# Performance work log

Hardware: AMD Instinct MI355X
Metric: run time of the kernel (lower is better)

Reference implementation:

```python
import jax, jax.numpy as jnp
import numpy as np

H = 3072; NH = 24; HD = 128; MLP_D = 12288
B = 1; IMG = 1536; REF = 512; TXT = 256

def _gelu_tanh(x):
    return jax.nn.gelu(x, approximate=True)

def _ln(x, eps=1e-6):
    m = jnp.mean(x, axis=-1, keepdims=True)
    v = jnp.var(x, axis=-1, keepdims=True)
    return (x - m) * jax.lax.rsqrt(v + eps)

def _rms(x, g, eps=1e-6):
    return x * jax.lax.rsqrt(jnp.mean(x * x, axis=-1, keepdims=True) + eps) * g

def _rot_half(x):
    # interleaved rotate-half: (x0,x1,x2,x3,...) -> (-x1,x0,-x3,x2,...)
    x2 = x.reshape(x.shape[:-1] + (-1, 2))
    return jnp.stack([-x2[..., 1], x2[..., 0]], axis=-1).reshape(x.shape)

def setup_inputs():
    key = jax.random.key(0)
    ks = jax.random.split(key, 16)
    s = 0.02
    # rope tables for image tokens (interleaved layout, values repeated x2)
    inv_freq = 1.0 / (10000.0 ** (jnp.arange(0, HD // 2, dtype=jnp.float32) / (HD // 2)))
    ang = jnp.arange(IMG, dtype=jnp.float32)[:, None] * inv_freq[None, :]   # [IMG, HD//2]
    ang = jnp.repeat(ang, 2, axis=-1)                                       # [IMG, HD]
    return {
        'x':   jax.random.normal(ks[0], (B, IMG + TXT, H), jnp.float32),
        'vec': jax.random.normal(ks[1], (B, H), jnp.float32),
        'ref': jax.random.normal(ks[2], (B, REF, H), jnp.float32),
        'cos': jnp.cos(ang), 'sin': jnp.sin(ang),
        'mod_w':  jax.random.normal(ks[3], (H, 3 * H), jnp.float32) * s,
        'mod_b':  jnp.zeros((3 * H,), jnp.float32),
        'rf1_w':  jax.random.normal(ks[4], (H, H), jnp.float32) * s,
        'rf1_b':  jnp.zeros((H,), jnp.float32),
        'rf2_w':  jax.random.normal(ks[5], (H, H), jnp.float32) * s,
        'rf2_b':  jnp.zeros((H,), jnp.float32),
        'rln_g':  jnp.ones((H,), jnp.float32),
        'rln_b':  jnp.zeros((H,), jnp.float32),
        'lin1_w': jax.random.normal(ks[6], (H, 3 * H + MLP_D), jnp.float32) * s,
        'lin1_b': jnp.zeros((3 * H + MLP_D,), jnp.float32),
        'q_g':    jnp.ones((HD,), jnp.float32),
        'k_g':    jnp.ones((HD,), jnp.float32),
        'lin2_w': jax.random.normal(ks[7], (H + MLP_D, H), jnp.float32) * s,
        'lin2_b': jnp.zeros((H,), jnp.float32),
        'text_mask': jnp.ones((B, TXT), jnp.int32),
        'img_len': IMG, 'txt_len': TXT,
    }

def _forward(x, vec, ref, cos, sin, mod_w, mod_b, rf1_w, rf1_b, rf2_w, rf2_b,
             rln_g, rln_b, lin1_w, lin1_b, q_g, k_g, lin2_w, lin2_b,
             text_mask, img_len, txt_len):
    Bb = x.shape[0]
    ref_len = ref.shape[1]
    # modulation (ModulateDiT: SiLU -> Linear -> chunk(3))
    mod = jnp.dot(jax.nn.silu(vec), mod_w) + mod_b
    shift, scale, gate = jnp.split(mod, 3, axis=-1)
    x_mod = _ln(x) * (1.0 + scale[:, None]) + shift[:, None]
    # ref MLP + affine LayerNorm
    r = jnp.dot(_gelu_tanh(jnp.dot(ref, rf1_w) + rf1_b), rf2_w) + rf2_b
    r = _ln(r) * rln_g + rln_b
    # token reassembly: [img | ref | txt]
    xc = jnp.concatenate([x_mod[:, :img_len], r, x_mod[:, img_len:]], axis=1)
    h = jnp.dot(xc, lin1_w) + lin1_b
    qkv, mlp = h[..., :3 * H], h[..., 3 * H:]
    L2 = xc.shape[1]
    q, k, v = [t.reshape(Bb, L2, NH, HD) for t in jnp.split(qkv, 3, axis=-1)]
    # q drops the ref span; ref contributes K/V only
    q = jnp.concatenate([q[:, :img_len], q[:, img_len + ref_len:]], axis=1)
    q = _rms(q, q_g)
    k = _rms(k, k_g)
    # rotary only on image tokens
    c = cos[None, :, None, :]; s = sin[None, :, None, :]
    img_q = q[:, :img_len] * c + _rot_half(q[:, :img_len]) * s
    img_k = k[:, :img_len] * c + _rot_half(k[:, :img_len]) * s
    q = jnp.concatenate([img_q, q[:, img_len:]], axis=1)          # [B, Lq, NH, HD]
    k = jnp.concatenate([img_k, k[:, img_len:]], axis=1)          # [B, Lkv, NH, HD]
    # varlen mask (cu_seqlens semantics): valid attends valid, pad attends pad
    tmask = text_mask.astype(bool)
    qv  = jnp.concatenate([jnp.ones((Bb, img_len), bool), tmask], axis=1)
    kvv = jnp.concatenate([jnp.ones((Bb, img_len + ref_len), bool), tmask], axis=1)
    allowed = (qv[:, None, :, None] == kvv[:, None, None, :])     # [B,1,Lq,Lkv]
    scores = jnp.einsum('bqhd,bkhd->bhqk', q, k) * (HD ** -0.5)
    scores = jnp.where(allowed, scores, jnp.asarray(-1e9, scores.dtype))
    p = jax.nn.softmax(scores, axis=-1)
    attn = jnp.einsum('bhqk,bkhd->bqhd', p, v).reshape(Bb, img_len + txt_len, H)
    mlp = jnp.concatenate([mlp[:, :img_len], mlp[:, img_len + ref_len:]], axis=1)
    out = jnp.dot(jnp.concatenate([attn, _gelu_tanh(mlp)], axis=-1), lin2_w) + lin2_b
    return x + out * gate[:, None]

def reference(x, vec, ref, cos, sin, mod_w, mod_b, rf1_w, rf1_b, rf2_w, rf2_b,
              rln_g, rln_b, lin1_w, lin1_b, q_g, k_g, lin2_w, lin2_b,
              text_mask, img_len, txt_len):
    return _forward(x, vec, ref, cos, sin, mod_w, mod_b, rf1_w, rf1_b, rf2_w, rf2_b,
                    rln_g, rln_b, lin1_w, lin1_b, q_g, k_g, lin2_w, lin2_b,
                    text_mask, img_len, txt_len)
```

## Files before the change

### kernel.cpp

```cpp
#include <hip/hip_runtime.h>
#include <cstdint>
#include <cstddef>

typedef unsigned short u16;
typedef unsigned int   u32;
typedef __bf16 bf16_t;
typedef bf16_t bf16x8 __attribute__((ext_vector_type(8)));
typedef float  f32x4  __attribute__((ext_vector_type(4)));
typedef u16    u16x4  __attribute__((ext_vector_type(4)));


__device__ __forceinline__ float b2f(u16 b){ u32 u=((u32)b)<<16; float f; __builtin_memcpy(&f,&u,4); return f; }
__device__ __forceinline__ u16 f2b(float f){ u32 u; __builtin_memcpy(&u,&f,4); u = u + 0x7fffu + ((u>>16)&1u); return (u16)(u>>16); }
__device__ __forceinline__ float gelu_f(float x){
  const float u2 = 1.5957691216057308f*(x + 0.044715f*x*x*x);
  return x/(1.f + __expf(-u2));
}

__device__ __forceinline__ void gload_lds16(const void* g, void* l){
  __builtin_amdgcn_global_load_lds((const __attribute__((address_space(1))) void*)g,
                                   (__attribute__((address_space(3))) void*)l, 16, 0, 0);
}

template<int NW, bool MX>
__device__ __forceinline__ float bred(float v, float* red){
  #pragma unroll
  for (int o=32;o;o>>=1){ float u=__shfl_down(v,o,64); v = MX? fmaxf(v,u) : v+u; }
  const int t = threadIdx.x;
  if ((t&63)==0) red[t>>6]=v;
  __syncthreads();
  float r = red[0];
  #pragma unroll
  for (int i=1;i<NW;i++) r = MX? fmaxf(r,red[i]) : r+red[i];
  __syncthreads();
  return r;
}

__device__ __forceinline__ void unpack8(uint4 u, float* f){
  f[0]=b2f((u16)(u.x&0xffffu)); f[1]=b2f((u16)(u.x>>16));
  f[2]=b2f((u16)(u.y&0xffffu)); f[3]=b2f((u16)(u.y>>16));
  f[4]=b2f((u16)(u.z&0xffffu)); f[5]=b2f((u16)(u.z>>16));
  f[6]=b2f((u16)(u.w&0xffffu)); f[7]=b2f((u16)(u.w>>16));
}
__device__ __forceinline__ uint4 pack8(const float* f){
  uint4 u;
  u.x = (u32)f2b(f[0]) | ((u32)f2b(f[1])<<16);
  u.y = (u32)f2b(f[2]) | ((u32)f2b(f[3])<<16);
  u.z = (u32)f2b(f[4]) | ((u32)f2b(f[5])<<16);
  u.w = (u32)f2b(f[6]) | ((u32)f2b(f[7])<<16);
  return u;
}

__global__ void modv_part(const float* __restrict__ vec, const float* __restrict__ W,
                          float* __restrict__ part){
  __shared__ float s[128];
  const int t = threadIdx.x;
  const int j = blockIdx.x*256 + t;
  const int i0 = blockIdx.y*128;
  if (t < 128){ float v = vec[i0+t]; s[t] = v/(1.f+__expf(-v)); }
  __syncthreads();
  float acc = 0.f;
  #pragma unroll 8
  for (int i=0;i<128;i++) acc += s[i]*W[(size_t)(i0+i)*9216 + j];
  part[(size_t)blockIdx.y*9216 + j] = acc;
}
__global__ void modv_reduce(const float* __restrict__ part, const float* __restrict__ mb,
                            float* __restrict__ modp){
  const int j = blockIdx.x*256 + threadIdx.x;
  float a = mb[j];
  #pragma unroll
  for (int c=0;c<24;c++) a += part[(size_t)c*9216 + j];
  modp[j] = a;
}

__global__ __launch_bounds__(256)
void convT(const float* __restrict__ W, u16* __restrict__ Wt, int Kd, int Nd){
  __shared__ float Ls[64][65];
  const int t = threadIdx.x;
  const int n0 = blockIdx.x*64, k0 = blockIdx.y*64;
  const int tr = t>>4;
  const int tc = (t&15)*4;
  #pragma unroll
  for (int p=0;p<4;p++){
    const int kk = tr + p*16;
    const float4 v = *(const float4*)(W + (size_t)(k0+kk)*Nd + n0 + tc);
    Ls[kk][tc+0]=v.x; Ls[kk][tc+1]=v.y; Ls[kk][tc+2]=v.z; Ls[kk][tc+3]=v.w;
  }
  __syncthreads();
  #pragma unroll
  for (int p=0;p<4;p++){
    const int nn = tr + p*16;
    u16x4 o;
    o.x = f2b(Ls[tc+0][nn]); o.y = f2b(Ls[tc+1][nn]);
    o.z = f2b(Ls[tc+2][nn]); o.w = f2b(Ls[tc+3][nn]);
    *(u16x4*)(Wt + (size_t)(n0+nn)*Kd + k0 + tc) = o;
  }
}

__global__ void convertF2B(const float* __restrict__ src, u16* __restrict__ dst){
  const size_t i = ((size_t)blockIdx.x*256 + threadIdx.x)*4;
  const float4 v = *(const float4*)(src+i);
  u16x4 o; o.x=f2b(v.x); o.y=f2b(v.y); o.z=f2b(v.z); o.w=f2b(v.w);
  *(u16x4*)(dst+i) = o;
}

__global__ void ln_modulate(const float* __restrict__ x, const float* __restrict__ modp,
                            u16* __restrict__ xc){
  __shared__ float red[4];
  const int row = blockIdx.x, t = threadIdx.x;
  const float* xr = x + (size_t)row*3072;
  float4 v[3]; float s=0.f, ss=0.f;
  #pragma unroll
  for (int k=0;k<3;k++){
    v[k] = *(const float4*)(xr + t*4 + k*1024);
    s  += v[k].x+v[k].y+v[k].z+v[k].w;
    ss += v[k].x*v[k].x+v[k].y*v[k].y+v[k].z*v[k].z+v[k].w*v[k].w;
  }
  s  = bred<4,false>(s, red);
  ss = bred<4,false>(ss, red);
  const float mean = s*(1.f/3072.f);
  const float inv = rsqrtf(ss*(1.f/3072.f)-mean*mean + 1e-6f);
  const int orow = row<1536 ? row : row+512;
  u16* o = xc + (size_t)orow*3072;
  const float* shiftp = modp; const float* scalep = modp+3072;
  #pragma unroll
  for (int k=0;k<3;k++){
    const int j = t*4 + k*1024;
    const float4 sc = *(const float4*)(scalep+j);
    const float4 sh = *(const float4*)(shiftp+j);
    u16x4 ov;
    ov.x = f2b((v[k].x-mean)*inv*(1.f+sc.x)+sh.x);
    ov.y = f2b((v[k].y-mean)*inv*(1.f+sc.y)+sh.y);
    ov.z = f2b((v[k].z-mean)*inv*(1.f+sc.z)+sh.z);
    ov.w = f2b((v[k].w-mean)*inv*(1.f+sc.w)+sh.w);
    *(u16x4*)(o+j) = ov;
  }
}

__global__ void ln_ref(const float* __restrict__ rt, const float* __restrict__ g,
                       const float* __restrict__ b, u16* __restrict__ xc){
  __shared__ float red[4];
  const int row = blockIdx.x, t = threadIdx.x;
  const float* xr = rt + (size_t)row*3072;
  float4 v[3]; float s=0.f, ss=0.f;
  #pragma unroll
  for (int k=0;k<3;k++){
    v[k] = *(const float4*)(xr + t*4 + k*1024);
    s  += v[k].x+v[k].y+v[k].z+v[k].w;
    ss += v[k].x*v[k].x+v[k].y*v[k].y+v[k].z*v[k].z+v[k].w*v[k].w;
  }
  s  = bred<4,false>(s, red);
  ss = bred<4,false>(ss, red);
  const float mean = s*(1.f/3072.f);
  const float inv = rsqrtf(ss*(1.f/3072.f)-mean*mean + 1e-6f);
  u16* o = xc + (size_t)(1536+row)*3072;
  #pragma unroll
  for (int k=0;k<3;k++){
    const int j = t*4 + k*1024;
    const float4 gv = *(const float4*)(g+j);
    const float4 bv = *(const float4*)(b+j);
    u16x4 ov;
    ov.x = f2b((v[k].x-mean)*inv*gv.x+bv.x);
    ov.y = f2b((v[k].y-mean)*inv*gv.y+bv.y);
    ov.z = f2b((v[k].z-mean)*inv*gv.z+bv.z);
    ov.w = f2b((v[k].w-mean)*inv*gv.w+bv.w);
    *(u16x4*)(o+j) = ov;
  }
}

__global__ void qk_prep(const u16* __restrict__ h, const float* __restrict__ qg,
                        const float* __restrict__ kg, const float* __restrict__ cosb,
                        const float* __restrict__ sinb, u16* __restrict__ Q,
                        u16* __restrict__ Kb){
  __shared__ float red[4];
  const int row = blockIdx.x, hd = blockIdx.y, d = threadIdx.x;
  const u16* hr = h + (size_t)row*21504;
  const float kv = b2f(hr[3072 + hd*128 + d]);
  const bool doq = (row < 1536) || (row >= 2048);
  const float qv = doq ? b2f(hr[hd*128 + d]) : 0.f;
  float a = kv*kv, b = qv*qv;
  #pragma unroll
  for (int o=32;o;o>>=1){ a += __shfl_down(a,o,64); b += __shfl_down(b,o,64); }
  if ((d&63)==0){ red[(d>>6)*2] = a; red[(d>>6)*2+1] = b; }
  __syncthreads();
  const float kinv = rsqrtf((red[0]+red[2])*(1.f/128.f) + 1e-6f);
  const float qinv = rsqrtf((red[1]+red[3])*(1.f/128.f) + 1e-6f);
  float kn = kv*kinv*kg[d];
  float qn = qv*qinv*qg[d];
  if (row < 1536){
    const float c  = cosb[row*128 + d];
    const float sn = sinb[row*128 + d];
    const float ko = b2f(hr[3072 + hd*128 + (d^1)])*kinv*kg[d^1];
    const float qo = b2f(hr[hd*128 + (d^1)])*qinv*qg[d^1];
    const float krh = (d&1) ? ko : -ko;
    const float qrh = (d&1) ? qo : -qo;
    kn = kn*c + krh*sn;
    qn = qn*c + qrh*sn;
  }
  Kb[((size_t)hd*2304 + row)*128 + d] = f2b(kn);
  if (doq){
    const int qrow = row<1536 ? row : row-512;
    Q[((size_t)hd*1792 + qrow)*128 + d] = f2b(qn);
  }
}

__global__ void v_transpose(const u16* __restrict__ h, u16* __restrict__ VT){
  __shared__ u16 Ls[32][33];
  const int tx = threadIdx.x, ty = threadIdx.y;
  const int l0 = blockIdx.x*32, d0 = blockIdx.y*32, hd = blockIdx.z;
  #pragma unroll
  for (int r=0;r<4;r++)
    Ls[ty+r*8][tx] = h[(size_t)(l0+ty+r*8)*21504 + 6144 + hd*128 + d0 + tx];
  __syncthreads();
  #pragma unroll
  for (int r=0;r<4;r++)
    VT[((size_t)hd*128 + d0+ty+r*8)*2304 + l0 + tx] = Ls[tx][ty+r*8];
}

__global__ void gelu_mlp(const u16* __restrict__ h, u16* __restrict__ out2){
  const int q = blockIdx.x;
  const int hrow = q<1536 ? q : q+512;
  const int j = blockIdx.y*2048 + threadIdx.x*8;
  const uint4 u = *(const uint4*)(h + (size_t)hrow*21504 + 9216 + j);
  float f[8]; unpack8(u, f);
  #pragma unroll
  for (int e=0;e<8;e++) f[e] = gelu_f(f[e]);
  const uint4 o = pack8(f);
  *(uint4*)(out2 + (size_t)q*15360 + 3072 + j) = o;
}

template<int EPI>
__global__ __launch_bounds__(256)
void gemm_bt(const u16* __restrict__ A, const u16* __restrict__ Bt,
             const float* __restrict__ bias, void* __restrict__ Cv,
             int K, int ldA, int ldB, int ldC,
             long long sA, long long sB, long long sC)
{
  __shared__ u16 As[128*32];
  __shared__ u16 Bs[128*32];
  const int t = threadIdx.x;
  const int w = t>>6, lane = t&63;
  const int bm = blockIdx.y, bn = blockIdx.x, bz = blockIdx.z;
  const u16* Ab = A + (size_t)((long long)bz*sA) + (size_t)bm*128*ldA;
  const u16* Bb = Bt + (size_t)((long long)bz*sB) + (size_t)bn*128*ldB;
  const int wm = w>>1, wn = w&1;
  const int lr = lane&15, lk = lane>>4;
  const int row0 = t>>2, kp0 = (t&3)*8;
  char* AsB = (char*)As; char* BsB = (char*)Bs;
  const int off0 = w*1024;
  const int off1 = 4096 + w*1024;
  f32x4 acc[4][4] = {};

  for (int kt = 0; kt < K; kt += 32){
    __syncthreads();
    gload_lds16(Ab + (size_t)row0*ldA + kt + kp0,      AsB + off0);
    gload_lds16(Ab + (size_t)(row0+64)*ldA + kt + kp0, AsB + off1);
    gload_lds16(Bb + (size_t)row0*ldB + kt + kp0,      BsB + off0);
    gload_lds16(Bb + (size_t)(row0+64)*ldB + kt + kp0, BsB + off1);
    __syncthreads();
    bf16x8 av[4], bv[4];
    #pragma unroll
    for (int i=0;i<4;i++) av[i] = *(const bf16x8*)(As + (wm*64+i*16+lr)*32 + lk*8);
    #pragma unroll
    for (int j=0;j<4;j++) bv[j] = *(const bf16x8*)(Bs + (wn*64+j*16+lr)*32 + lk*8);
    #pragma unroll
    for (int i=0;i<4;i++)
      #pragma unroll
      for (int j=0;j<4;j++)
        acc[i][j] = __builtin_amdgcn_mfma_f32_16x16x32_bf16(av[i], bv[j], acc[i][j], 0,0,0);
  }

  const int mBase = bm*128 + wm*64;
  const int nBase = bn*128 + wn*64;
  #pragma unroll
  for (int i=0;i<4;i++){
    #pragma unroll
    for (int j=0;j<4;j++){
      #pragma unroll
      for (int r=0;r<4;r++){
        const int m = mBase + i*16 + lk*4 + r;
        const int n = nBase + j*16 + lr;
        const float v = acc[i][j][r];
        const long long idx = (long long)bz*sC + (long long)m*ldC + n;
        if (EPI==6){
          ((float*)Cv)[idx] = v;
        } else {
          ((u16*)Cv)[idx] = f2b(v + bias[n]);
        }
      }
    }
  }
}

__global__ void comb_gelu(const float* __restrict__ P, const float* __restrict__ b,
                          u16* __restrict__ o){
  const size_t e = ((size_t)blockIdx.x*256 + threadIdx.x)*4;
  const int n = (int)(e % 3072);
  const size_t S = (size_t)512*3072;
  float4 a = *(const float4*)(P + e);
  #pragma unroll
  for (int c=1;c<6;c++){
    const float4 p = *(const float4*)(P + c*S + e);
    a.x+=p.x; a.y+=p.y; a.z+=p.z; a.w+=p.w;
  }
  const float4 bb = *(const float4*)(b + n);
  u16x4 ov;
  ov.x = f2b(gelu_f(a.x+bb.x)); ov.y = f2b(gelu_f(a.y+bb.y));
  ov.z = f2b(gelu_f(a.z+bb.z)); ov.w = f2b(gelu_f(a.w+bb.w));
  *(u16x4*)(o + e) = ov;
}
__global__ void comb_bias(const float* __restrict__ P, const float* __restrict__ b,
                          float* __restrict__ o){
  const size_t e = ((size_t)blockIdx.x*256 + threadIdx.x)*4;
  const int n = (int)(e % 3072);
  const size_t S = (size_t)512*3072;
  float4 a = *(const float4*)(P + e);
  #pragma unroll
  for (int c=1;c<6;c++){
    const float4 p = *(const float4*)(P + c*S + e);
    a.x+=p.x; a.y+=p.y; a.z+=p.z; a.w+=p.w;
  }
  const float4 bb = *(const float4*)(b + n);
  float4 ov; ov.x=a.x+bb.x; ov.y=a.y+bb.y; ov.z=a.z+bb.z; ov.w=a.w+bb.w;
  *(float4*)(o + e) = ov;
}

#define G256_BAR()  __builtin_amdgcn_s_barrier()
#define G256_LGKM() do{ asm volatile("s_waitcnt lgkmcnt(0)" ::: "memory"); \
                        __builtin_amdgcn_sched_barrier(0); }while(0)

template<int CEPI>
__global__ __launch_bounds__(512,2)
void gemm256(const u16* __restrict__ A, const u16* __restrict__ Bt,
             const float* __restrict__ bias, void* __restrict__ Cv,
             int Kc, int ld, int ldC, int nbn, int ntile, long long sC, int nwg, int gm)
{
  __shared__ char smem[131072];
  const int t = threadIdx.x;
  const int wid = t>>6, lane = t&63;
  const int lr = lane&15, lk = lane>>4;
  const int wm = wid>>2, wn = wid&3;

  const int orig = blockIdx.x;
  const int q8 = nwg>>3, r8 = nwg&7;
  const int xcd = orig&7, jj = orig>>3;
  const int wg = (xcd<r8 ? xcd*(q8+1) : r8*(q8+1) + (xcd-r8)*q8) + jj;
  int sk, bm, bn;
  if (gm > 0){
    const int band = wg / (gm*nbn);
    const int rr = wg - band*(gm*nbn);
    bn = rr / gm;
    bm = band*gm + (rr - bn*gm);
    sk = 0;
  } else {
    sk = wg / ntile;
    const int rem = wg - sk*ntile;
    bm = rem / nbn; bn = rem % nbn;
  }

  const u16* Agl = A  + (size_t)bm*256*ld + (size_t)sk*Kc;
  const u16* Bgl = Bt + (size_t)bn*256*ld + (size_t)sk*Kc;
  const int NT = Kc>>6;

  const int d0 = wid*64 + lane;
  const int sr = d0>>3;
  const size_t soff = (size_t)sr*ld + (size_t)(((d0&7)^(sr&7))<<3);

  const int xsl0 = ((lk    ) ^ (lr&7))<<4;
  const int xsl1 = ((lk | 4) ^ (lr&7))<<4;

  f32x4 acc[8][4] = {};
  bf16x8 bv[4][2];

  auto STAGE = [&](const u16* g, int h, int kt, char* ldsMat){
    const u16* s0 = g + (size_t)(h*128)*ld + kt + soff;
    char* l0 = ldsMat + h*16384 + wid*1024;
    gload_lds16(s0, l0);
    gload_lds16(s0 + (size_t)64*ld, l0 + 8192);
  };

  STAGE(Agl, 0, 0, smem);
  STAGE(Agl, 1, 0, smem);
  STAGE(Bgl, 0, 0, smem + 32768);
  STAGE(Bgl, 1, 0, smem + 32768);
  if (NT > 1){
    STAGE(Bgl, 0, 64, smem + 65536 + 32768);
    STAGE(Bgl, 1, 64, smem + 65536 + 32768);
    asm volatile("s_waitcnt vmcnt(4)" ::: "memory");
  } else {
    asm volatile("s_waitcnt vmcnt(0)" ::: "memory");
  }
  G256_BAR();

#define G256_MFMA_Q(Q)                                                          \
  do{                                                                           \
    _Pragma("unroll")                                                           \
    for (int j=0;j<4;j++){                                                      \
      acc[(Q)*2+0][j] = __builtin_amdgcn_mfma_f32_16x16x32_bf16(av00, bv[j][0], acc[(Q)*2+0][j], 0,0,0); \
      acc[(Q)*2+0][j] = __builtin_amdgcn_mfma_f32_16x16x32_bf16(av01, bv[j][1], acc[(Q)*2+0][j], 0,0,0); \
      acc[(Q)*2+1][j] = __builtin_amdgcn_mfma_f32_16x16x32_bf16(av10, bv[j][0], acc[(Q)*2+1][j], 0,0,0); \
      acc[(Q)*2+1][j] = __builtin_amdgcn_mfma_f32_16x16x32_bf16(av11, bv[j][1], acc[(Q)*2+1][j], 0,0,0); \
    }                                                                           \
  }while(0)

#define G256_PHASE(Q, STG, TAILW)                                               \
  do{                                                                           \
    const char* abase = cA + (wm*128 + (Q)*32 + lr)*128;                        \
    bf16x8 av00 = *(const bf16x8*)(abase + xsl0);                               \
    bf16x8 av01 = *(const bf16x8*)(abase + xsl1);                               \
    bf16x8 av10 = *(const bf16x8*)(abase + 2048 + xsl0);                        \
    bf16x8 av11 = *(const bf16x8*)(abase + 2048 + xsl1);                        \
    if ((Q)==0){                                                                \
      _Pragma("unroll")                                                         \
      for (int j=0;j<4;j++){                                                    \
        const char* bbase = cB + (wn*64 + j*16 + lr)*128;                       \
        bv[j][0] = *(const bf16x8*)(bbase + xsl0);                              \
        bv[j][1] = *(const bf16x8*)(bbase + xsl1);                              \
      }                                                                         \
    }                                                                           \
    STG;                                                                        \
    G256_BAR();                                                                 \
    G256_LGKM();                                                                \
    __builtin_amdgcn_s_setprio(1);                                              \
    G256_MFMA_Q(Q);                                                             \
    __builtin_amdgcn_s_setprio(0);                                              \
    TAILW;                                                                      \
    G256_BAR();                                                                 \
  }while(0)

  for (int tt = 0; tt < NT; ++tt){
    char* cA = smem + (tt&1)*65536;
    char* cB = cA + 32768;
    char* nA = smem + ((tt+1)&1)*65536;
    const int kt1 = (tt+1)<<6, kt2 = (tt+2)<<6;
    const bool stA = (tt+1) < NT, stB = (tt+2) < NT;

    G256_PHASE(0, if (stA) STAGE(Agl, 0, kt1, nA), );
    G256_PHASE(1, if (stA) STAGE(Agl, 1, kt1, nA), );
    G256_PHASE(2, if (stB) STAGE(Bgl, 0, kt2, cB), );
    G256_PHASE(3, if (stB) STAGE(Bgl, 1, kt2, cB),
               if (stB)      { asm volatile("s_waitcnt vmcnt(4)" ::: "memory"); }
               else if (stA) { asm volatile("s_waitcnt vmcnt(0)" ::: "memory"); } );
  }
#undef G256_PHASE
#undef G256_MFMA_Q

  const int mB = bm*256 + wm*128 + lk*4;
  const int nB = bn*256 + wn*64 + lr;
  #pragma unroll
  for (int fi=0; fi<8; fi++){
    #pragma unroll
    for (int j=0; j<4; j++){
      const int n = nB + j*16;
      const float bb = (CEPI==0) ? bias[n] : 0.f;
      #pragma unroll
      for (int r=0;r<4;r++){
        const int m = mB + fi*16 + r;
        if (CEPI==0){
          ((u16*)Cv)[(size_t)m*ldC + n] = f2b(acc[fi][j][r] + bb);
        } else {
          ((float*)Cv)[(size_t)sk*sC + (size_t)m*ldC + n] = acc[fi][j][r];
        }
      }
    }
  }
}

__global__ __launch_bounds__(512)
void flash_attn(const u16* __restrict__ Qb, const u16* __restrict__ Kb,
                const u16* __restrict__ VT, const int* __restrict__ tmask,
                u16* __restrict__ out2)
{
  __shared__ __attribute__((aligned(16))) char smf[81920];
  char* Ks0 = smf;
  char* Vs0 = smf + 32768;
  char* Ps  = smf + 65536;
  const int t = threadIdx.x, wid = t>>6, lane = t&63;
  const int lr = lane&15, hi = lane>>4;
  const int head = blockIdx.y, qt = blockIdx.x;
  const int q0 = qt*128;
  const u16* Qg = Qb + ((size_t)head*1792 + q0)*128;
  const u16* Kg = Kb + (size_t)head*2304*128;
  const u16* Vg = VT + (size_t)head*128*2304;
  const float SCALE = 0.08838834764831845f;

  u32 kbits = 0;
  #pragma unroll
  for (int i=0;i<16;i++) kbits |= (u32)(tmask[i*16 + lr] != 0) << i;
  int fqr[4];
  #pragma unroll
  for (int r=0;r<4;r++){
    const int q = q0 + wid*16 + hi*4 + r;
    fqr[r] = (q < 1536) ? 1 : (tmask[q-1536] != 0);
  }

  #pragma unroll
  for (int c=0;c<4;c++){
    const int s = c*512 + wid*64 + lane;
    const int row = s>>4, dsl = s&15;
    gload_lds16(Qg + (size_t)row*128 + ((dsl ^ (row&7))<<3),
                Vs0 + (size_t)(c*512 + wid*64)*16);
  }
  #pragma unroll
  for (int c=0;c<2;c++){
    const int s = c*512 + wid*64 + lane;
    const int row = s>>4, dsl = s&15;
    gload_lds16(Kg + (size_t)row*128 + ((dsl ^ (row&7))<<3),
                Ks0 + (size_t)(c*512 + wid*64)*16);
  }
  asm volatile("s_waitcnt vmcnt(0)" ::: "memory");
  __syncthreads();

  bf16x8 av[4];
  {
    const int row = wid*16 + lr;
    #pragma unroll
    for (int ks=0;ks<4;ks++)
      av[ks] = *(const bf16x8*)(Vs0 + row*256 + (((ks*4+hi) ^ (row&7))<<4));
  }
  asm volatile("s_waitcnt lgkmcnt(0)" ::: "memory");
  __builtin_amdgcn_sched_barrier(0);
  __syncthreads();

  #pragma unroll
  for (int c=0;c<2;c++){
    const int s = c*512 + wid*64 + lane;
    const int row = s>>3, dsl = s&7;
    gload_lds16(Vg + (size_t)row*2304 + ((dsl ^ (row&7))<<3),
                Vs0 + (size_t)(c*512 + wid*64)*16);
  }
  asm volatile("s_waitcnt vmcnt(0)" ::: "memory");
  __syncthreads();

  f32x4 acc[8] = {};
  float m_[4], l_[4];
  #pragma unroll
  for (int r=0;r<4;r++){ m_[r] = -3e38f; l_[r] = 0.f; }

  for (int kt = 0; kt < 36; ++kt){
    char* Kc = Ks0 + (kt&1)*16384;
    char* Vc = Vs0 + (kt&1)*16384;
    if (kt+1 < 36){
      char* Kn = Ks0 + ((kt+1)&1)*16384;
      char* Vn = Vs0 + ((kt+1)&1)*16384;
      #pragma unroll
      for (int c=0;c<2;c++){
        const int s = c*512 + wid*64 + lane;
        { const int row = s>>4, dsl = s&15;
          gload_lds16(Kg + (size_t)((kt+1)*64 + row)*128 + ((dsl ^ (row&7))<<3),
                      Kn + (size_t)(c*512 + wid*64)*16); }
        { const int row = s>>3, dsl = s&7;
          gload_lds16(Vg + (size_t)row*2304 + (kt+1)*64 + ((dsl ^ (row&7))<<3),
                      Vn + (size_t)(c*512 + wid*64)*16); }
      }
    }
    f32x4 sacc[4] = {};
    #pragma unroll
    for (int ks=0;ks<4;ks++){
      #pragma unroll
      for (int j=0;j<4;j++){
        const int row = j*16 + lr;
        bf16x8 bk = *(const bf16x8*)(Kc + row*256 + (((ks*4+hi) ^ (row&7))<<4));
        sacc[j] = __builtin_amdgcn_mfma_f32_16x16x32_bf16(av[ks], bk, sacc[j], 0,0,0);
      }
    }
    int gkj[4];
    #pragma unroll
    for (int j=0;j<4;j++)
      gkj[j] = (kt < 32) ? 1 : (int)((kbits >> ((kt-32)*4 + j)) & 1u);
    float p[4][4]; bool alw[4][4];
    float mt[4] = {-3e38f,-3e38f,-3e38f,-3e38f};
    #pragma unroll
    for (int j=0;j<4;j++){
      #pragma unroll
      for (int r=0;r<4;r++){
        const float s = sacc[j][r]*SCALE;
        const bool a = (fqr[r] == gkj[j]);
        alw[j][r] = a; p[j][r] = s;
        if (a) mt[r] = fmaxf(mt[r], s);
      }
    }
    #pragma unroll
    for (int r=0;r<4;r++){
      #pragma unroll
      for (int o=1;o<16;o<<=1) mt[r] = fmaxf(mt[r], __shfl_xor(mt[r], o, 64));
      const float nm = fmaxf(m_[r], mt[r]);
      const float cr = __expf(m_[r] - nm);
      m_[r] = nm;
      l_[r] *= cr;
      #pragma unroll
      for (int jp=0;jp<8;jp++) acc[jp][r] *= cr;
    }
    float rs[4] = {0.f,0.f,0.f,0.f};
    #pragma unroll
    for (int j=0;j<4;j++){
      #pragma unroll
      for (int r=0;r<4;r++){
        const float pv = alw[j][r] ? __expf(p[j][r] - m_[r]) : 0.f;
        p[j][r] = pv; rs[r] += pv;
      }
    }
    #pragma unroll
    for (int r=0;r<4;r++){
      #pragma unroll
      for (int o=1;o<16;o<<=1) rs[r] += __shfl_xor(rs[r], o, 64);
      l_[r] += rs[r];
    }
    #pragma unroll
    for (int j=0;j<4;j++){
      #pragma unroll
      for (int r=0;r<4;r++){
        const int q = wid*16 + hi*4 + r;
        const int k = j*16 + lr;
        *(u16*)(Ps + q*128 + (((k>>3) ^ (q&7))<<4) + (k&7)*2) = f2b(p[j][r]);
      }
    }
    asm volatile("s_waitcnt lgkmcnt(0)" ::: "memory");
    __builtin_amdgcn_sched_barrier(0);
    bf16x8 pa[2];
    {
      const int row = wid*16 + lr;
      #pragma unroll
      for (int ks2=0;ks2<2;ks2++)
        pa[ks2] = *(const bf16x8*)(Ps + row*128 + (((ks2*4+hi) ^ (row&7))<<4));
    }
    #pragma unroll
    for (int ks2=0;ks2<2;ks2++){
      #pragma unroll
      for (int jp=0;jp<8;jp++){
        const int row = jp*16 + lr;
        bf16x8 bvv = *(const bf16x8*)(Vc + row*128 + (((ks2*4+hi) ^ (row&7))<<4));
        acc[jp] = __builtin_amdgcn_mfma_f32_16x16x32_bf16(pa[ks2], bvv, acc[jp], 0,0,0);
      }
    }
    asm volatile("s_waitcnt vmcnt(0)" ::: "memory");
    __syncthreads();
  }

  float inv[4];
  #pragma unroll
  for (int r=0;r<4;r++) inv[r] = 1.f/l_[r];
  #pragma unroll
  for (int jp=0;jp<8;jp++){
    #pragma unroll
    for (int r=0;r<4;r++){
      const size_t q = q0 + wid*16 + hi*4 + r;
      out2[q*15360 + head*128 + jp*16 + lr] = f2b(acc[jp][r]*inv[r]);
    }
  }
}

__global__ void lin2_fin(const float* __restrict__ P, const float* __restrict__ x,
                         const float* __restrict__ bias, const float* __restrict__ gate,
                         float* __restrict__ out){
  const size_t e = ((size_t)blockIdx.x*256 + threadIdx.x)*4;
  const int n = (int)(e % 3072);
  const size_t S = (size_t)1792*3072;
  float4 a = *(const float4*)(P + e);
  #pragma unroll
  for (int c=1;c<6;c++){
    const float4 p = *(const float4*)(P + c*S + e);
    a.x+=p.x; a.y+=p.y; a.z+=p.z; a.w+=p.w;
  }
  const float4 bb = *(const float4*)(bias + n);
  const float4 gg = *(const float4*)(gate + n);
  const float4 xv = *(const float4*)(x + e);
  float4 o;
  o.x = xv.x + (a.x+bb.x)*gg.x;
  o.y = xv.y + (a.y+bb.y)*gg.y;
  o.z = xv.z + (a.z+bb.z)*gg.z;
  o.w = xv.w + (a.w+bb.w)*gg.w;
  *(float4*)(out + e) = o;
}

extern "C" void kernel_launch(void* const* d_in, const int* in_sizes, int n_in,
                              void* d_out, int out_size, void* d_ws, size_t ws_size,
                              hipStream_t stream)
{
  (void)in_sizes; (void)n_in; (void)out_size; (void)ws_size;
  const float* x     = (const float*)d_in[0];
  const float* vec   = (const float*)d_in[1];
  const float* ref   = (const float*)d_in[2];
  const float* cosb  = (const float*)d_in[3];
  const float* sinb  = (const float*)d_in[4];
  const float* mod_w = (const float*)d_in[5];
  const float* mod_b = (const float*)d_in[6];
  const float* rf1_w = (const float*)d_in[7];
  const float* rf1_b = (const float*)d_in[8];
  const float* rf2_w = (const float*)d_in[9];
  const float* rf2_b = (const float*)d_in[10];
  const float* rln_g = (const float*)d_in[11];
  const float* rln_b = (const float*)d_in[12];
  const float* lin1_w= (const float*)d_in[13];
  const float* lin1_b= (const float*)d_in[14];
  const float* q_g   = (const float*)d_in[15];
  const float* k_g   = (const float*)d_in[16];
  const float* lin2_w= (const float*)d_in[17];
  const float* lin2_b= (const float*)d_in[18];
  const int*   tmask = (const int*)d_in[19];
  float* out = (float*)d_out;
  char* ws = (char*)d_ws;

  float* modp = (float*)(ws + 0);
  float* part = (float*)(ws + 36864);
  u16*  w2t   = (u16*)(ws + 921600);
  u16*  Qb    = (u16*)(ws + 95293440ll);
  u16*  Kb    = (u16*)(ws + 106303488ll);
  u16*  VT    = (u16*)(ws + 120459264ll);
  u16*  out2  = (u16*)(ws + 134615040ll);
  u16*  w1t   = (u16*)(ws + 189665280ll);
  u16*  xc    = (u16*)(ws + 321785856ll);
  u16*  rf1t  = (u16*)(ws + 335941632ll);
  u16*  rf2t  = (u16*)(ws + 354816000ll);
  u16*  refb  = (u16*)(ws + 373690368ll);
  u16*  tb    = (u16*)(ws + 376836096ll);
  float* rtmp = (float*)(ws + 379981824ll);
  float* rp   = (float*)(ws + 386273280ll);
  u16*  hbuf  = (u16*)(ws + 335941632ll);
  float* p2b  = (float*)(ws + 189665280ll);

  modv_part<<<dim3(36,24),256,0,stream>>>(vec, mod_w, part);
  modv_reduce<<<36,256,0,stream>>>(part, mod_b, modp);
  convT<<<dim3(48,48),  256,0,stream>>>(rf1_w, rf1t, 3072, 3072);
  convT<<<dim3(48,48),  256,0,stream>>>(rf2_w, rf2t, 3072, 3072);
  convT<<<dim3(336,48), 256,0,stream>>>(lin1_w, w1t, 3072, 21504);
  convT<<<dim3(48,240), 256,0,stream>>>(lin2_w, w2t, 15360, 3072);
  convertF2B<<<1536,256,0,stream>>>(ref, refb);
  ln_modulate<<<1792,256,0,stream>>>(x, modp, xc);
  gemm_bt<6><<<dim3(24,4,6),256,0,stream>>>(refb, rf1t, nullptr, rp, 512, 3072,3072,3072,
                                            512,512, (long long)512*3072);
  comb_gelu<<<1536,256,0,stream>>>(rp, rf1_b, tb);
  gemm_bt<6><<<dim3(24,4,6),256,0,stream>>>(tb, rf2t, nullptr, rp, 512, 3072,3072,3072,
                                            512,512, (long long)512*3072);
  comb_bias<<<1536,256,0,stream>>>(rp, rf2_b, rtmp);
  ln_ref<<<512,256,0,stream>>>(rtmp, rln_g, rln_b, xc);
  gemm256<0><<<756,512,0,stream>>>(xc, w1t, lin1_b, hbuf, 3072, 3072, 21504, 84, 756, 0, 756, 3);
  gelu_mlp<<<dim3(1792,6),256,0,stream>>>(hbuf, out2);
  qk_prep<<<dim3(2304,24),128,0,stream>>>(hbuf, q_g, k_g, cosb, sinb, Qb, Kb);
  v_transpose<<<dim3(72,4,24),dim3(32,8),0,stream>>>(hbuf, VT);
  flash_attn<<<dim3(14,24),512,0,stream>>>(Qb, Kb, VT, tmask, out2);
  gemm256<1><<<504,512,0,stream>>>(out2, w2t, nullptr, p2b, 2560, 15360, 3072, 12, 84,
                                   (long long)1792*3072, 504, 0);
  lin2_fin<<<5376,256,0,stream>>>(p2b, x, lin2_b, modp + 6144, out);
}
```

Baseline: 923.7 us.

## Merge GEMM k-loop into two phases and bound flash_attn occupancy

Restructures the 256x256 GEMM main loop from four phases (each with two barriers) into two phases that each load two A sub-tiles and issue both A stages or both B stages at once, halving the barrier count per k-step. It also adds a min-blocks hint of 4 to the flash_attention launch bounds. The merged phases hold more A fragments live, which raises register pressure. The launch-bounds hint may force register spilling in the attention kernel.

```diff
diff --git a/kernel.cpp b/kernel.cpp
--- a/kernel.cpp
+++ b/kernel.cpp
@@ -392,42 +392,6 @@
   }
   G256_BAR();
 
-#define G256_MFMA_Q(Q)                                                          \
-  do{                                                                           \
-    _Pragma("unroll")                                                           \
-    for (int j=0;j<4;j++){                                                      \
-      acc[(Q)*2+0][j] = __builtin_amdgcn_mfma_f32_16x16x32_bf16(av00, bv[j][0], acc[(Q)*2+0][j], 0,0,0); \
-      acc[(Q)*2+0][j] = __builtin_amdgcn_mfma_f32_16x16x32_bf16(av01, bv[j][1], acc[(Q)*2+0][j], 0,0,0); \
-      acc[(Q)*2+1][j] = __builtin_amdgcn_mfma_f32_16x16x32_bf16(av10, bv[j][0], acc[(Q)*2+1][j], 0,0,0); \
-      acc[(Q)*2+1][j] = __builtin_amdgcn_mfma_f32_16x16x32_bf16(av11, bv[j][1], acc[(Q)*2+1][j], 0,0,0); \
-    }                                                                           \
-  }while(0)
-
-#define G256_PHASE(Q, STG, TAILW)                                               \
-  do{                                                                           \
-    const char* abase = cA + (wm*128 + (Q)*32 + lr)*128;                        \
-    bf16x8 av00 = *(const bf16x8*)(abase + xsl0);                               \
-    bf16x8 av01 = *(const bf16x8*)(abase + xsl1);                               \
-    bf16x8 av10 = *(const bf16x8*)(abase + 2048 + xsl0);                        \
-    bf16x8 av11 = *(const bf16x8*)(abase + 2048 + xsl1);                        \
-    if ((Q)==0){                                                                \
-      _Pragma("unroll")                                                         \
-      for (int j=0;j<4;j++){                                                    \
-        const char* bbase = cB + (wn*64 + j*16 + lr)*128;                       \
-        bv[j][0] = *(const bf16x8*)(bbase + xsl0);                              \
-        bv[j][1] = *(const bf16x8*)(bbase + xsl1);                              \
-      }                                                                         \
-    }                                                                           \
-    STG;                                                                        \
-    G256_BAR();                                                                 \
-    G256_LGKM();                                                                \
-    __builtin_amdgcn_s_setprio(1);                                              \
-    G256_MFMA_Q(Q);                                                             \
-    __builtin_amdgcn_s_setprio(0);                                              \
-    TAILW;                                                                      \
-    G256_BAR();                                                                 \
-  }while(0)
-
   for (int tt = 0; tt < NT; ++tt){
     char* cA = smem + (tt&1)*65536;
     char* cB = cA + 32768;
@@ -435,15 +399,73 @@
     const int kt1 = (tt+1)<<6, kt2 = (tt+2)<<6;
     const bool stA = (tt+1) < NT, stB = (tt+2) < NT;
 
-    G256_PHASE(0, if (stA) STAGE(Agl, 0, kt1, nA), );
-    G256_PHASE(1, if (stA) STAGE(Agl, 1, kt1, nA), );
-    G256_PHASE(2, if (stB) STAGE(Bgl, 0, kt2, cB), );
-    G256_PHASE(3, if (stB) STAGE(Bgl, 1, kt2, cB),
-               if (stB)      { asm volatile("s_waitcnt vmcnt(4)" ::: "memory"); }
-               else if (stA) { asm volatile("s_waitcnt vmcnt(0)" ::: "memory"); } );
-  }
-#undef G256_PHASE
-#undef G256_MFMA_Q
+    {
+      const char* ab0 = cA + (wm*128 + 0*32 + lr)*128;
+      const char* ab1 = cA + (wm*128 + 1*32 + lr)*128;
+      bf16x8 a00 = *(const bf16x8*)(ab0 + xsl0);
+      bf16x8 a01 = *(const bf16x8*)(ab0 + xsl1);
+      bf16x8 a02 = *(const bf16x8*)(ab0 + 2048 + xsl0);
+      bf16x8 a03 = *(const bf16x8*)(ab0 + 2048 + xsl1);
+      bf16x8 a10 = *(const bf16x8*)(ab1 + xsl0);
+      bf16x8 a11 = *(const bf16x8*)(ab1 + xsl1);
+      bf16x8 a12 = *(const bf16x8*)(ab1 + 2048 + xsl0);
+      bf16x8 a13 = *(const bf16x8*)(ab1 + 2048 + xsl1);
+      #pragma unroll
+      for (int j=0;j<4;j++){
+        const char* bbase = cB + (wn*64 + j*16 + lr)*128;
+        bv[j][0] = *(const bf16x8*)(bbase + xsl0);
+        bv[j][1] = *(const bf16x8*)(bbase + xsl1);
+      }
+      if (stA){ STAGE(Agl, 0, kt1, nA); STAGE(Agl, 1, kt1, nA); }
+      G256_BAR();
+      G256_LGKM();
+      __builtin_amdgcn_s_setprio(1);
+      #pragma unroll
+      for (int j=0;j<4;j++){
+        acc[0][j] = __builtin_amdgcn_mfma_f32_16x16x32_bf16(a00, bv[j][0], acc[0][j], 0,0,0);
+        acc[0][j] = __builtin_amdgcn_mfma_f32_16x16x32_bf16(a01, bv[j][1], acc[0][j], 0,0,0);
+        acc[1][j] = __builtin_amdgcn_mfma_f32_16x16x32_bf16(a02, bv[j][0], acc[1][j], 0,0,0);
+        acc[1][j] = __builtin_amdgcn_mfma_f32_16x16x32_bf16(a03, bv[j][1], acc[1][j], 0,0,0);
+        acc[2][j] = __builtin_amdgcn_mfma_f32_16x16x32_bf16(a10, bv[j][0], acc[2][j], 0,0,0);
+        acc[2][j] = __builtin_amdgcn_mfma_f32_16x16x32_bf16(a11, bv[j][1], acc[2][j], 0,0,0);
+        acc[3][j] = __builtin_amdgcn_mfma_f32_16x16x32_bf16(a12, bv[j][0], acc[3][j], 0,0,0);
+        acc[3][j] = __builtin_amdgcn_mfma_f32_16x16x32_bf16(a13, bv[j][1], acc[3][j], 0,0,0);
+      }
+      __builtin_amdgcn_s_setprio(0);
+      G256_BAR();
+    }
+    {
+      const char* ab2 = cA + (wm*128 + 2*32 + lr)*128;
+      const char* ab3 = cA + (wm*128 + 3*32 + lr)*128;
+      bf16x8 a20 = *(const bf16x8*)(ab2 + xsl0);
+      bf16x8 a21 = *(const bf16x8*)(ab2 + xsl1);
+      bf16x8 a22 = *(const bf16x8*)(ab2 + 2048 + xsl0);
+      bf16x8 a23 = *(const bf16x8*)(ab2 + 2048 + xsl1);
+      bf16x8 a30 = *(const bf16x8*)(ab3 + xsl0);
+      bf16x8 a31 = *(const bf16x8*)(ab3 + xsl1);
+      bf16x8 a32 = *(const bf16x8*)(ab3 + 2048 + xsl0);
+      bf16x8 a33 = *(const bf16x8*)(ab3 + 2048 + xsl1);
+      if (stB){ STAGE(Bgl, 0, kt2, cB); STAGE(Bgl, 1, kt2, cB); }
+      G256_BAR();
+      G256_LGKM();
+      __builtin_amdgcn_s_setprio(1);
+      #pragma unroll
+      for (int j=0;j<4;j++){
+        acc[4][j] = __builtin_amdgcn_mfma_f32_16x16x32_bf16(a20, bv[j][0], acc[4][j], 0,0,0);
+        acc[4][j] = __builtin_amdgcn_mfma_f32_16x16x32_bf16(a21, bv[j][1], acc[4][j], 0,0,0);
+        acc[5][j] = __builtin_amdgcn_mfma_f32_16x16x32_bf16(a22, bv[j][0], acc[5][j], 0,0,0);
+        acc[5][j] = __builtin_amdgcn_mfma_f32_16x16x32_bf16(a23, bv[j][1], acc[5][j], 0,0,0);
+        acc[6][j] = __builtin_amdgcn_mfma_f32_16x16x32_bf16(a30, bv[j][0], acc[6][j], 0,0,0);
+        acc[6][j] = __builtin_amdgcn_mfma_f32_16x16x32_bf16(a31, bv[j][1], acc[6][j], 0,0,0);
+        acc[7][j] = __builtin_amdgcn_mfma_f32_16x16x32_bf16(a32, bv[j][0], acc[7][j], 0,0,0);
+        acc[7][j] = __builtin_amdgcn_mfma_f32_16x16x32_bf16(a33, bv[j][1], acc[7][j], 0,0,0);
+      }
+      __builtin_amdgcn_s_setprio(0);
+      if (stB)      { asm volatile("s_waitcnt vmcnt(4)" ::: "memory"); }
+      else if (stA) { asm volatile("s_waitcnt vmcnt(0)" ::: "memory"); }
+      G256_BAR();
+    }
+  }
 
   const int mB = bm*256 + wm*128 + lk*4;
   const int nB = bn*256 + wn*64 + lr;
@@ -466,7 +488,7 @@
   }
 }
 
-__global__ __launch_bounds__(512)
+__global__ __launch_bounds__(512,4)
 void flash_attn(const u16* __restrict__ Qb, const u16* __restrict__ Kb,
                 const u16* __restrict__ VT, const int* __restrict__ tmask,
                 u16* __restrict__ out2)
```

Result: no change. 906.6 us (-1.8%).

## Skip unused lin1 tiles for ref rows and unroll GEMM K-loop by two

Applied to the files above, without the earlier changes.

Adds a custom tile map for the lin1 GEMM. For the reference-token row blocks it launches only the column tiles that produce K and V, skipping the Q and MLP outputs that are later discarded. This cuts the grid from 756 to 636 workgroups. The gemm256 main loop is also unrolled over two K-steps with fixed LDS buffer pointers, which removes per-iteration buffer address arithmetic but assumes an even number of K tiles. flash_attn gets a min-blocks hint of 4 in its launch bounds, which may constrain register allocation.

```diff
diff --git a/kernel.cpp b/kernel.cpp
--- a/kernel.cpp
+++ b/kernel.cpp
@@ -328,6 +328,20 @@
 #define G256_BAR()  __builtin_amdgcn_s_barrier()
 #define G256_LGKM() do{ asm volatile("s_waitcnt lgkmcnt(0)" ::: "memory"); \
                         __builtin_amdgcn_sched_barrier(0); }while(0)
+#define G256_VM4()  asm volatile("s_waitcnt vmcnt(4)" ::: "memory")
+#define G256_VM0()  asm volatile("s_waitcnt vmcnt(0)" ::: "memory")
+
+__device__ __forceinline__ void lin1_map(int tw, int& bm, int& bn){
+  if (tw < 504){
+    const int band = tw/252; const int rr = tw - band*252;
+    bn = rr/3; bm = band*3 + (rr - bn*3);
+  } else if (tw < 588){
+    bm = 8; bn = tw - 504;
+  } else {
+    const int rem = tw - 588;
+    bm = 6 + (rem&1); bn = 12 + (rem>>1);
+  }
+}
 
 template<int CEPI>
 __global__ __launch_bounds__(512,2)
@@ -346,7 +360,9 @@
   const int xcd = orig&7, jj = orig>>3;
   const int wg = (xcd<r8 ? xcd*(q8+1) : r8*(q8+1) + (xcd-r8)*q8) + jj;
   int sk, bm, bn;
-  if (gm > 0){
+  if (gm == -1){
+    sk = 0; lin1_map(wg, bm, bn);
+  } else if (gm > 0){
     const int band = wg / (gm*nbn);
     const int rr = wg - band*(gm*nbn);
     bn = rr / gm;
@@ -361,13 +377,18 @@
   const u16* Agl = A  + (size_t)bm*256*ld + (size_t)sk*Kc;
   const u16* Bgl = Bt + (size_t)bn*256*ld + (size_t)sk*Kc;
   const int NT = Kc>>6;
+  const int NI = NT>>1;
 
   const int d0 = wid*64 + lane;
   const int sr = d0>>3;
   const size_t soff = (size_t)sr*ld + (size_t)(((d0&7)^(sr&7))<<3);
-
   const int xsl0 = ((lk    ) ^ (lr&7))<<4;
   const int xsl1 = ((lk | 4) ^ (lr&7))<<4;
+
+  char* s0A = smem;
+  char* s0B = smem + 32768;
+  char* s1A = smem + 65536;
+  char* s1B = smem + 98304;
 
   f32x4 acc[8][4] = {};
   bf16x8 bv[4][2];
@@ -379,71 +400,62 @@
     gload_lds16(s0 + (size_t)64*ld, l0 + 8192);
   };
 
-  STAGE(Agl, 0, 0, smem);
-  STAGE(Agl, 1, 0, smem);
-  STAGE(Bgl, 0, 0, smem + 32768);
-  STAGE(Bgl, 1, 0, smem + 32768);
-  if (NT > 1){
-    STAGE(Bgl, 0, 64, smem + 65536 + 32768);
-    STAGE(Bgl, 1, 64, smem + 65536 + 32768);
-    asm volatile("s_waitcnt vmcnt(4)" ::: "memory");
-  } else {
-    asm volatile("s_waitcnt vmcnt(0)" ::: "memory");
-  }
+  STAGE(Agl, 0, 0, s0A);
+  STAGE(Agl, 1, 0, s0A);
+  STAGE(Bgl, 0, 0, s0B);
+  STAGE(Bgl, 1, 0, s0B);
+  STAGE(Bgl, 0, 64, s1B);
+  STAGE(Bgl, 1, 64, s1B);
+  G256_VM4();
   G256_BAR();
 
-#define G256_MFMA_Q(Q)                                                          \
+#define G256_PH(SA, Q, READB, SB, STG, TAILV)                                   \
   do{                                                                           \
-    _Pragma("unroll")                                                           \
-    for (int j=0;j<4;j++){                                                      \
-      acc[(Q)*2+0][j] = __builtin_amdgcn_mfma_f32_16x16x32_bf16(av00, bv[j][0], acc[(Q)*2+0][j], 0,0,0); \
-      acc[(Q)*2+0][j] = __builtin_amdgcn_mfma_f32_16x16x32_bf16(av01, bv[j][1], acc[(Q)*2+0][j], 0,0,0); \
-      acc[(Q)*2+1][j] = __builtin_amdgcn_mfma_f32_16x16x32_bf16(av10, bv[j][0], acc[(Q)*2+1][j], 0,0,0); \
-      acc[(Q)*2+1][j] = __builtin_amdgcn_mfma_f32_16x16x32_bf16(av11, bv[j][1], acc[(Q)*2+1][j], 0,0,0); \
-    }                                                                           \
-  }while(0)
-
-#define G256_PHASE(Q, STG, TAILW)                                               \
-  do{                                                                           \
-    const char* abase = cA + (wm*128 + (Q)*32 + lr)*128;                        \
-    bf16x8 av00 = *(const bf16x8*)(abase + xsl0);                               \
-    bf16x8 av01 = *(const bf16x8*)(abase + xsl1);                               \
-    bf16x8 av10 = *(const bf16x8*)(abase + 2048 + xsl0);                        \
-    bf16x8 av11 = *(const bf16x8*)(abase + 2048 + xsl1);                        \
-    if ((Q)==0){                                                                \
+    const char* ab = SA + (wm*128 + (Q)*32 + lr)*128;                           \
+    bf16x8 a0 = *(const bf16x8*)(ab + xsl0);                                    \
+    bf16x8 a1 = *(const bf16x8*)(ab + xsl1);                                    \
+    bf16x8 a2 = *(const bf16x8*)(ab + 2048 + xsl0);                             \
+    bf16x8 a3 = *(const bf16x8*)(ab + 2048 + xsl1);                             \
+    if (READB){                                                                 \
       _Pragma("unroll")                                                         \
       for (int j=0;j<4;j++){                                                    \
-        const char* bbase = cB + (wn*64 + j*16 + lr)*128;                       \
-        bv[j][0] = *(const bf16x8*)(bbase + xsl0);                              \
-        bv[j][1] = *(const bf16x8*)(bbase + xsl1);                              \
+        const char* bb = SB + (wn*64 + j*16 + lr)*128;                          \
+        bv[j][0] = *(const bf16x8*)(bb + xsl0);                                 \
+        bv[j][1] = *(const bf16x8*)(bb + xsl1);                                 \
       }                                                                         \
     }                                                                           \
     STG;                                                                        \
     G256_BAR();                                                                 \
     G256_LGKM();                                                                \
     __builtin_amdgcn_s_setprio(1);                                              \
-    G256_MFMA_Q(Q);                                                             \
+    _Pragma("unroll")                                                           \
+    for (int j=0;j<4;j++){                                                      \
+      acc[(Q)*2+0][j] = __builtin_amdgcn_mfma_f32_16x16x32_bf16(a0, bv[j][0], acc[(Q)*2+0][j], 0,0,0); \
+      acc[(Q)*2+0][j] = __builtin_amdgcn_mfma_f32_16x16x32_bf16(a1, bv[j][1], acc[(Q)*2+0][j], 0,0,0); \
+      acc[(Q)*2+1][j] = __builtin_amdgcn_mfma_f32_16x16x32_bf16(a2, bv[j][0], acc[(Q)*2+1][j], 0,0,0); \
+      acc[(Q)*2+1][j] = __builtin_amdgcn_mfma_f32_16x16x32_bf16(a3, bv[j][1], acc[(Q)*2+1][j], 0,0,0); \
+    }                                                                           \
     __builtin_amdgcn_s_setprio(0);                                              \
-    TAILW;                                                                      \
+    TAILV;                                                                      \
     G256_BAR();                                                                 \
   }while(0)
 
-  for (int tt = 0; tt < NT; ++tt){
-    char* cA = smem + (tt&1)*65536;
-    char* cB = cA + 32768;
-    char* nA = smem + ((tt+1)&1)*65536;
-    const int kt1 = (tt+1)<<6, kt2 = (tt+2)<<6;
-    const bool stA = (tt+1) < NT, stB = (tt+2) < NT;
-
-    G256_PHASE(0, if (stA) STAGE(Agl, 0, kt1, nA), );
-    G256_PHASE(1, if (stA) STAGE(Agl, 1, kt1, nA), );
-    G256_PHASE(2, if (stB) STAGE(Bgl, 0, kt2, cB), );
-    G256_PHASE(3, if (stB) STAGE(Bgl, 1, kt2, cB),
-               if (stB)      { asm volatile("s_waitcnt vmcnt(4)" ::: "memory"); }
-               else if (stA) { asm volatile("s_waitcnt vmcnt(0)" ::: "memory"); } );
-  }
-#undef G256_PHASE
-#undef G256_MFMA_Q
+  for (int it2 = 0; it2 < NI; ++it2){
+    const int t0 = it2*2;
+    const bool s2 = (t0+2) < NT, s3 = (t0+3) < NT;
+    const int k1 = (t0+1)<<6, k2 = (t0+2)<<6, k3 = (t0+3)<<6;
+
+    G256_PH(s0A, 0, 1, s0B, { STAGE(Agl,0,k1,s1A); STAGE(Agl,1,k1,s1A); }, );
+    G256_PH(s0A, 1, 0, s0B, if (s2) STAGE(Bgl,0,k2,s0B), );
+    G256_PH(s0A, 2, 0, s0B, if (s2) STAGE(Bgl,1,k2,s0B), );
+    G256_PH(s0A, 3, 0, s0B, , if (s2) G256_VM4(); else G256_VM0(); );
+    G256_PH(s1A, 0, 1, s1B, if (s2) STAGE(Agl,0,k2,s0A), );
+    G256_PH(s1A, 1, 0, s1B, if (s2) STAGE(Agl,1,k2,s0A), );
+    G256_PH(s1A, 2, 0, s1B, if (s3) STAGE(Bgl,0,k3,s1B), );
+    G256_PH(s1A, 3, 0, s1B, if (s3) STAGE(Bgl,1,k3,s1B),
+            if (s3) G256_VM4(); else G256_VM0(); );
+  }
+#undef G256_PH
 
   const int mB = bm*256 + wm*128 + lk*4;
   const int nB = bn*256 + wn*64 + lr;
@@ -466,7 +478,7 @@
   }
 }
 
-__global__ __launch_bounds__(512)
+__global__ __launch_bounds__(512,4)
 void flash_attn(const u16* __restrict__ Qb, const u16* __restrict__ Kb,
                 const u16* __restrict__ VT, const int* __restrict__ tmask,
                 u16* __restrict__ out2)
@@ -734,7 +746,7 @@
                                             512,512, (long long)512*3072);
   comb_bias<<<1536,256,0,stream>>>(rp, rf2_b, rtmp);
   ln_ref<<<512,256,0,stream>>>(rtmp, rln_g, rln_b, xc);
-  gemm256<0><<<756,512,0,stream>>>(xc, w1t, lin1_b, hbuf, 3072, 3072, 21504, 84, 756, 0, 756, 3);
+  gemm256<0><<<636,512,0,stream>>>(xc, w1t, lin1_b, hbuf, 3072, 3072, 21504, 84, 636, 0, 636, -1);
   gelu_mlp<<<dim3(1792,6),256,0,stream>>>(hbuf, out2);
   qk_prep<<<dim3(2304,24),128,0,stream>>>(hbuf, q_g, k_g, cosb, sinb, Qb, Kb);
   v_transpose<<<dim3(72,4,24),dim3(32,8),0,stream>>>(hbuf, VT);
```

After: 900.1 us. -2.6%, faster.
